# Optimization experiments

Hardware: AMD Instinct MI355X
Metric: run time of the kernel (lower is better)

## Reference

```python
import jax, jax.numpy as jnp
import numpy as np

B = 1          # batch
CAM = 6        # num cameras
HW = 256       # tokens per camera (16x16 latent)
N = CAM * HW   # 1536 image tokens
D = 1024       # model dim
H = 16         # heads
DH = 64        # dim_head
L = 4          # depth
V = 8192       # image token vocab
VC = 4096      # cond vocab
NC = 512       # num cond tokens
INNER = int(D * 4 * 2 / 3)  # 2730 GEGLU inner dim
SCALE = 8.0


def setup_inputs() -> dict:
    key = jax.random.key(0)
    ks = jax.random.split(key, 24)
    w = lambda k, shape: jax.random.normal(k, shape, jnp.float32) * 0.02
    inp = {
        'x': jax.random.randint(ks[0], (B * CAM, HW), 0, V),
        'cond_ids': jax.random.randint(ks[1], (B, NC), 0, VC),
        'token_emb': w(ks[2], (V, D)),
        'pos_emb': w(ks[3], (N, D)),
        'cond_token_emb': w(ks[4], (VC, D)),
        'cond_pos_emb': w(ks[5], (NC, D)),
        # self-attention (per layer, stacked on leading L axis)
        'sa_g': jnp.ones((L, D), jnp.float32),
        'sa_wq': w(ks[6], (L, D, H * DH)),
        'sa_wkv': w(ks[7], (L, D, 2 * H * DH)),
        'sa_null': jax.random.normal(ks[8], (L, 2, H, 1, DH), jnp.float32),
        'sa_qs': jnp.ones((L, DH), jnp.float32),
        'sa_ks': jnp.ones((L, DH), jnp.float32),
        'sa_wo': w(ks[9], (L, H * DH, D)),
        # cross-attention
        'ca_g': jnp.ones((L, D), jnp.float32),
        'ca_wq': w(ks[10], (L, D, H * DH)),
        'ca_wkv': w(ks[11], (L, D, 2 * H * DH)),
        'ca_null': jax.random.normal(ks[12], (L, 2, H, 1, DH), jnp.float32),
        'ca_qs': jnp.ones((L, DH), jnp.float32),
        'ca_ks': jnp.ones((L, DH), jnp.float32),
        'ca_wo': w(ks[13], (L, H * DH, D)),
        # GEGLU feedforward
        'ff_g1': jnp.ones((L, D), jnp.float32),
        'ff_w1': w(ks[14], (L, D, 2 * INNER)),
        'ff_g2': jnp.ones((L, INNER), jnp.float32),
        'ff_w2': w(ks[15], (L, INNER, D)),
        'final_g': jnp.ones((D,), jnp.float32),
        'w_logits': w(ks[16], (D, V)),
    }
    return inp


def _ln(x, g):
    m = jnp.mean(x, axis=-1, keepdims=True)
    v = jnp.var(x, axis=-1, keepdims=True)
    return (x - m) * jax.lax.rsqrt(v + 1e-5) * g


def _l2n(x):
    n = jnp.sqrt(jnp.sum(x * x, axis=-1, keepdims=True))
    return x / jnp.maximum(n, 1e-12)


def _attn(x, kv, g, wq, wkv, nkv, qs, ks_, wo):
    b, n, _ = x.shape
    xn = _ln(x, g)
    kv_in = xn if kv is None else kv  # cross-attn uses raw context (not normed)
    q = (xn @ wq) * SCALE  # matches torch (no-op after l2norm, kept faithful)
    k, v = jnp.split(kv_in @ wkv, 2, axis=-1)
    to_h = lambda t: t.reshape(b, -1, H, DH).transpose(0, 2, 1, 3)  # b h n d
    q, k, v = to_h(q), to_h(k), to_h(v)
    nk = jnp.broadcast_to(nkv[0], (b, H, 1, DH))
    nv = jnp.broadcast_to(nkv[1], (b, H, 1, DH))
    k = jnp.concatenate([nk, k], axis=2)
    v = jnp.concatenate([nv, v], axis=2)
    q = _l2n(q) * qs
    k = _l2n(k) * ks_
    sim = jnp.einsum('bhid,bhjd->bhij', q, k) * SCALE
    a = jax.nn.softmax(sim, axis=-1)
    o = jnp.einsum('bhij,bhjd->bhid', a, v)
    return o.transpose(0, 2, 1, 3).reshape(b, n, H * DH) @ wo


def _ff(x, g1, w1, g2, w2):
    h = _ln(x, g1) @ w1
    a, gate = jnp.split(h, 2, axis=-1)
    h = gate * jax.nn.gelu(a, approximate=False)  # GEGLU, exact gelu like torch
    return _ln(h, g2) @ w2


def reference(x, cond_ids, token_emb, pos_emb, cond_token_emb, cond_pos_emb,
              sa_g, sa_wq, sa_wkv, sa_null, sa_qs, sa_ks, sa_wo,
              ca_g, ca_wq, ca_wkv, ca_null, ca_qs, ca_ks, ca_wo,
              ff_g1, ff_w1, ff_g2, ff_w2, final_g, w_logits):
    h = token_emb[x].reshape(B, N, D) + pos_emb[:N]
    ctx = cond_token_emb[cond_ids] + cond_pos_emb[:NC]
    layer_params = (sa_g, sa_wq, sa_wkv, sa_null, sa_qs, sa_ks, sa_wo,
                    ca_g, ca_wq, ca_wkv, ca_null, ca_qs, ca_ks, ca_wo,
                    ff_g1, ff_w1, ff_g2, ff_w2)

    def body(h, p):
        (sg, swq, swkv, snull, sqs, sks, swo,
         cg, cwq, cwkv, cnull, cqs, cks, cwo,
         fg1, fw1, fg2, fw2) = p
        h = h + _attn(h, None, sg, swq, swkv, snull, sqs, sks, swo)
        h = h + _attn(h, ctx, cg, cwq, cwkv, cnull, cqs, cks, cwo)
        h = h + _ff(h, fg1, fw1, fg2, fw2)
        return h, None

    h, _ = jax.lax.scan(body, h, layer_params)
    h = _ln(h, final_g)  # TransformerBlocks.norm
    return h @ w_logits  # (B, N, V)
```

## Files before the change

### kernel.cpp

```cpp
#include <hip/hip_runtime.h>

typedef __attribute__((ext_vector_type(8))) short short8;
typedef __attribute__((ext_vector_type(4))) float f32x4;
typedef unsigned short u16;

#define N_TOK   1536
#define DMODEL  1024
#define NHEAD   16
#define DHEAD   64
#define NCTX    512
#define INNERD  2730
#define INNERP  2752
#define FF1P    5504
#define VOCAB   8192

__device__ __forceinline__ u16 f2b(float f) {
  union { float f; unsigned u; } v; v.f = f;
  unsigned r = (v.u >> 16) & 1u;
  return (u16)((v.u + 0x7fffu + r) >> 16);
}

__global__ __launch_bounds__(256) void conv_t(
    const float* __restrict__ in, u16* __restrict__ out,
    int K, int Nw, int Kpad, int Nbound, long long zin, long long zout)
{
  const float* inl = in + (size_t)blockIdx.z * zin;
  u16* outl = out + (size_t)blockIdx.z * zout;
  __shared__ float tile[64][65];
  int k0 = blockIdx.x * 64, n0 = blockIdx.y * 64;
  int tid = threadIdx.x;
  {
    int r = tid >> 4, c4 = (tid & 15) * 4;
#pragma unroll
    for (int j = 0; j < 4; j++) {
      int k = k0 + r + j * 16;
      float4 v = make_float4(0.f, 0.f, 0.f, 0.f);
      if (k < K && (n0 + c4) < Nw) v = *(const float4*)&inl[(size_t)k * Nw + n0 + c4];
      tile[r + j * 16][c4] = v.x; tile[r + j * 16][c4 + 1] = v.y;
      tile[r + j * 16][c4 + 2] = v.z; tile[r + j * 16][c4 + 3] = v.w;
    }
  }
  __syncthreads();
  {
    int nl = tid >> 2, kc = (tid & 3) * 16;
    int n = n0 + nl;
    if (n < Nbound) {
      u16 pk[16];
#pragma unroll
      for (int i = 0; i < 16; i++) pk[i] = f2b(tile[kc + i][nl]);
      u16* op = outl + (size_t)n * Kpad + k0 + kc;
      *(short8*)&op[0] = *(short8*)&pk[0];
      *(short8*)&op[8] = *(short8*)&pk[8];
    }
  }
}

__global__ void embed_img(const int* __restrict__ x, const float* __restrict__ temb,
                          const float* __restrict__ pemb, float* __restrict__ h) {
  int n = blockIdx.x; int tok = x[n]; int d4 = threadIdx.x;
  float4 a = *(const float4*)&temb[(size_t)tok * DMODEL + d4 * 4];
  float4 b = *(const float4*)&pemb[(size_t)n * DMODEL + d4 * 4];
  float4 o; o.x = a.x + b.x; o.y = a.y + b.y; o.z = a.z + b.z; o.w = a.w + b.w;
  *(float4*)&h[(size_t)n * DMODEL + d4 * 4] = o;
}

__global__ void embed_ctx(const int* __restrict__ ids, const float* __restrict__ temb,
                          const float* __restrict__ pemb, u16* __restrict__ ctxb) {
  int n = blockIdx.x; int tok = ids[n]; int d4 = threadIdx.x;
  float4 a = *(const float4*)&temb[(size_t)tok * DMODEL + d4 * 4];
  float4 b = *(const float4*)&pemb[(size_t)n * DMODEL + d4 * 4];
  u16* o = ctxb + (size_t)n * DMODEL + d4 * 4;
  o[0] = f2b(a.x + b.x); o[1] = f2b(a.y + b.y); o[2] = f2b(a.z + b.z); o[3] = f2b(a.w + b.w);
}

__global__ __launch_bounds__(256) void ln_bf16(
    const float* __restrict__ X, int ldin, const float* __restrict__ g,
    u16* __restrict__ Y, int ldout, int C, int Cpad)
{
  int row = blockIdx.x;
  const float* x = X + (size_t)row * ldin;
  float s = 0.f, sq = 0.f;
  for (int ci = threadIdx.x; ci < C; ci += 256) { float v = x[ci]; s += v; sq += v * v; }
#pragma unroll
  for (int m = 1; m < 64; m <<= 1) { s += __shfl_xor(s, m, 64); sq += __shfl_xor(sq, m, 64); }
  __shared__ float red[2][4];
  int w = threadIdx.x >> 6;
  if ((threadIdx.x & 63) == 0) { red[0][w] = s; red[1][w] = sq; }
  __syncthreads();
  s = red[0][0] + red[0][1] + red[0][2] + red[0][3];
  sq = red[1][0] + red[1][1] + red[1][2] + red[1][3];
  float mean = s / C;
  float var = sq / C - mean * mean;
  float rstd = rsqrtf(var + 1e-5f);
  u16* y = Y + (size_t)row * ldout;
  for (int ci = threadIdx.x; ci < C; ci += 256) y[ci] = f2b((x[ci] - mean) * rstd * g[ci]);
  for (int ci = C + threadIdx.x; ci < Cpad; ci += 256) y[ci] = 0;
}

template <int WMODE, int NSPLIT>
__global__ __launch_bounds__(256) void gemm_bt(
    const u16* __restrict__ A, const u16* __restrict__ Bt,
    float* __restrict__ C, int ldc, int M, int N, int K, int lda, int ldb)
{
  __shared__ __align__(16) short As[128 * 72];
  __shared__ __align__(16) short Bs[128 * 72];
  int tid = threadIdx.x;
  int bm = blockIdx.x, bn = blockIdx.y;
  int lane = tid & 63, w = tid >> 6;
  int wm = (w >> 1) * 64, wn = (w & 1) * 64;
  int rl = lane & 15, quad = lane >> 4;
  f32x4 acc[4][4];
#pragma unroll
  for (int i = 0; i < 4; i++)
#pragma unroll
    for (int j = 0; j < 4; j++) acc[i][j] = (f32x4)(0.f);
  const int rowA0 = bm * 128, rowB0 = bn * 128;
  int tiles = K >> 6;
  int t0 = (tiles * blockIdx.z) / NSPLIT, t1 = (tiles * (blockIdx.z + 1)) / NSPLIT;

  for (int kt = t0; kt < t1; kt++) {
    int k0 = kt * 64;
    __syncthreads();
#pragma unroll
    for (int i = 0; i < 4; i++) {
      int ch = tid + 256 * i;
      int r = ch >> 3, c8 = (ch & 7) * 8;
      *(short8*)&As[r * 72 + c8] = *(const short8*)(A + (size_t)(rowA0 + r) * lda + k0 + c8);
      *(short8*)&Bs[r * 72 + c8] = *(const short8*)(Bt + (size_t)(rowB0 + r) * ldb + k0 + c8);
    }
    __syncthreads();
#pragma unroll
    for (int kk = 0; kk < 64; kk += 32) {
      int kq = kk + quad * 8;
      short8 af[4], bfr[4];
#pragma unroll
      for (int t = 0; t < 4; t++) {
        af[t]  = *(const short8*)&As[(wm + t * 16 + rl) * 72 + kq];
        bfr[t] = *(const short8*)&Bs[(wn + t * 16 + rl) * 72 + kq];
      }
#pragma unroll
      for (int mt = 0; mt < 4; mt++)
#pragma unroll
        for (int nt = 0; nt < 4; nt++)
          acc[mt][nt] = __builtin_amdgcn_mfma_f32_16x16x32_bf16(af[mt], bfr[nt], acc[mt][nt], 0, 0, 0);
    }
  }
#pragma unroll
  for (int mt = 0; mt < 4; mt++)
#pragma unroll
    for (int nt = 0; nt < 4; nt++)
#pragma unroll
      for (int r = 0; r < 4; r++) {
        int row = rowA0 + wm + mt * 16 + quad * 4 + r;
        int col = rowB0 + wn + nt * 16 + rl;
        float* p = &C[(size_t)row * ldc + col];
        if (WMODE == 0) *p = acc[mt][nt][r];
        else if (WMODE == 1) *p += acc[mt][nt][r];
        else atomicAdd(p, acc[mt][nt][r]);
      }
}

__global__ __launch_bounds__(256) void prep_kv(
    const float* __restrict__ kvb,
    const float* __restrict__ nullkv, const float* __restrict__ ks,
    u16* __restrict__ Kn, u16* __restrict__ Vt, int Lk, int Lkp)
{
  int h = blockIdx.y, j0 = blockIdx.x * 64;
  int tid = threadIdx.x, w = tid >> 6, d = tid & 63;
  float ksd = ks[d];
#pragma unroll 4
  for (int r = 0; r < 16; r++) {
    int j = j0 + w * 16 + r;
    float k = 0.f;
    if (j == 0) k = nullkv[h * 64 + d];
    else if (j < Lk) k = kvb[(size_t)(j - 1) * 3072 + h * 64 + d];
    float ssq = k * k;
#pragma unroll
    for (int ms = 1; ms < 64; ms <<= 1) ssq += __shfl_xor(ssq, ms, 64);
    float kn = k * (1.0f / fmaxf(sqrtf(ssq), 1e-12f)) * ksd;
    Kn[((size_t)h * Lkp + j) * 64 + d] = f2b(kn);
  }
  __shared__ float tile[64][65];
  {
    int jl = tid >> 2, c16 = (tid & 3) * 16;
    int j = j0 + jl;
#pragma unroll
    for (int i4 = 0; i4 < 4; i4++) {
      float4 v = make_float4(0.f, 0.f, 0.f, 0.f);
      if (j == 0) v = *(const float4*)&nullkv[NHEAD * 64 + h * 64 + c16 + i4 * 4];
      else if (j < Lk) v = *(const float4*)&kvb[(size_t)(j - 1) * 3072 + 1024 + h * 64 + c16 + i4 * 4];
      tile[jl][c16 + i4 * 4] = v.x; tile[jl][c16 + i4 * 4 + 1] = v.y;
      tile[jl][c16 + i4 * 4 + 2] = v.z; tile[jl][c16 + i4 * 4 + 3] = v.w;
    }
  }
  __syncthreads();
  {
    int dd = tid >> 2, jc = (tid & 3) * 16;
    u16 pk[16];
#pragma unroll
    for (int i = 0; i < 16; i++) pk[i] = f2b(tile[jc + i][dd]);
    u16* op = Vt + ((size_t)h * 64 + dd) * Lkp + j0 + jc;
    *(short8*)&op[0] = *(short8*)&pk[0];
    *(short8*)&op[8] = *(short8*)&pk[8];
  }
}

__global__ __launch_bounds__(256) void attn_mfma(
    const float* __restrict__ qkv, const float* __restrict__ qs,
    const u16* __restrict__ Kn, const u16* __restrict__ Vt,
    float* __restrict__ Opar, float* __restrict__ Lpar, int Lkp, int nk)
{
  __shared__ __align__(16) u16 Kt[2][64 * 64];
  __shared__ __align__(16) u16 Vs[2][64 * 64];
  __shared__ __align__(16) short Ps[4 * 16 * 72];
  int tid = threadIdx.x, w = tid >> 6, lane = tid & 63;
  int rl = lane & 15, quad = lane >> 4;
  int b = blockIdx.x;
  int h = (b & 7) * 2 + ((b >> 3) & 1);
  int rest = b >> 4;
  int qg = rest >> 1, ks = rest & 1;
  int m0 = qg * 64 + w * 16;
  int t0 = (nk * ks) >> 1, t1 = (nk * (ks + 1)) >> 1;
  short* Pw = Ps + w * 16 * 72;

  short8 aq[2];
  {
    const float* qp = qkv + (size_t)(m0 + rl) * 3072 + h * 64;
    float qv[16];
    float ssq = 0.f;
#pragma unroll
    for (int cb = 0; cb < 2; cb++) {
      float4 v0 = *(const float4*)&qp[cb * 32 + quad * 8];
      float4 v1 = *(const float4*)&qp[cb * 32 + quad * 8 + 4];
      qv[cb * 8 + 0] = v0.x; qv[cb * 8 + 1] = v0.y; qv[cb * 8 + 2] = v0.z; qv[cb * 8 + 3] = v0.w;
      qv[cb * 8 + 4] = v1.x; qv[cb * 8 + 5] = v1.y; qv[cb * 8 + 6] = v1.z; qv[cb * 8 + 7] = v1.w;
      ssq += v0.x * v0.x + v0.y * v0.y + v0.z * v0.z + v0.w * v0.w;
      ssq += v1.x * v1.x + v1.y * v1.y + v1.z * v1.z + v1.w * v1.w;
    }
    ssq += __shfl_xor(ssq, 16, 64);
    ssq += __shfl_xor(ssq, 32, 64);
    float inv = 8.0f / fmaxf(sqrtf(ssq), 1e-12f);
    u16 pk[16];
#pragma unroll
    for (int cb = 0; cb < 2; cb++) {
      float4 s0 = *(const float4*)&qs[cb * 32 + quad * 8];
      float4 s1 = *(const float4*)&qs[cb * 32 + quad * 8 + 4];
      pk[cb * 8 + 0] = f2b(qv[cb * 8 + 0] * inv * s0.x);
      pk[cb * 8 + 1] = f2b(qv[cb * 8 + 1] * inv * s0.y);
      pk[cb * 8 + 2] = f2b(qv[cb * 8 + 2] * inv * s0.z);
      pk[cb * 8 + 3] = f2b(qv[cb * 8 + 3] * inv * s0.w);
      pk[cb * 8 + 4] = f2b(qv[cb * 8 + 4] * inv * s1.x);
      pk[cb * 8 + 5] = f2b(qv[cb * 8 + 5] * inv * s1.y);
      pk[cb * 8 + 6] = f2b(qv[cb * 8 + 6] * inv * s1.z);
      pk[cb * 8 + 7] = f2b(qv[cb * 8 + 7] * inv * s1.w);
    }
    aq[0] = *(short8*)&pk[0];
    aq[1] = *(short8*)&pk[8];
  }

  const u16* Kh = Kn + (size_t)h * Lkp * 64;
  const u16* Vh = Vt + (size_t)h * 64 * Lkp;

  int srow0 = w * 16 + (lane >> 3);
  int scol = (lane & 7) * 8;

  short8 stg[4];
  {
    int j0 = t0 * 64;
#pragma unroll
    for (int c = 0; c < 2; c++) {
      int row = srow0 + c * 8;
      stg[c]     = *(const short8*)(Kh + (size_t)(j0 + row) * 64 + scol);
      stg[2 + c] = *(const short8*)(Vh + (size_t)row * Lkp + j0 + scol);
    }
  }

  f32x4 oacc[4];
#pragma unroll
  for (int dt = 0; dt < 4; dt++) oacc[dt] = (f32x4)(0.f);
  float lrow[4] = {0.f, 0.f, 0.f, 0.f};

  for (int kt = t0; kt < t1; kt++) {
    int buf = kt & 1;
    u16* KtB = Kt[buf];
    u16* VsB = Vs[buf];
#pragma unroll
    for (int c = 0; c < 2; c++) {
      int row = srow0 + c * 8;
      int cs = scol ^ ((row & 7) * 8);
      *(short8*)&KtB[row * 64 + cs] = stg[c];
      *(short8*)&VsB[row * 64 + cs] = stg[2 + c];
    }
    if (kt + 1 < t1) {
      int j0 = (kt + 1) * 64;
#pragma unroll
      for (int c = 0; c < 2; c++) {
        int row = srow0 + c * 8;
        stg[c]     = *(const short8*)(Kh + (size_t)(j0 + row) * 64 + scol);
        stg[2 + c] = *(const short8*)(Vh + (size_t)row * Lkp + j0 + scol);
      }
    }
    __asm volatile("s_waitcnt lgkmcnt(0)" ::: "memory");
    __builtin_amdgcn_s_barrier();
    __asm volatile("" ::: "memory");

    f32x4 sacc[4];
#pragma unroll
    for (int nt = 0; nt < 4; nt++) sacc[nt] = (f32x4)(0.f);
#pragma unroll
    for (int kc = 0; kc < 2; kc++)
#pragma unroll
      for (int nt = 0; nt < 4; nt++) {
        short8 bkf = *(const short8*)&KtB[(nt * 16 + rl) * 64 + (((kc * 4 + quad) ^ (rl & 7)) * 8)];
        sacc[nt] = __builtin_amdgcn_mfma_f32_16x16x32_bf16(aq[kc], bkf, sacc[nt], 0, 0, 0);
      }

#pragma unroll
    for (int nt = 0; nt < 4; nt++)
#pragma unroll
      for (int r = 0; r < 4; r++) {
        float p = __expf(sacc[nt][r]);
        lrow[r] += p;
        Pw[(quad * 4 + r) * 72 + nt * 16 + rl] = (short)f2b(p);
      }
    __asm volatile("s_waitcnt lgkmcnt(0)" ::: "memory");
    short8 ap0 = *(const short8*)&Pw[rl * 72 + quad * 8];
    short8 ap1 = *(const short8*)&Pw[rl * 72 + 32 + quad * 8];
#pragma unroll
    for (int dt = 0; dt < 4; dt++) {
      short8 bv0 = *(const short8*)&VsB[(dt * 16 + rl) * 64 + ((quad ^ (rl & 7)) * 8)];
      short8 bv1 = *(const short8*)&VsB[(dt * 16 + rl) * 64 + (((4 + quad) ^ (rl & 7)) * 8)];
      oacc[dt] = __builtin_amdgcn_mfma_f32_16x16x32_bf16(ap0, bv0, oacc[dt], 0, 0, 0);
      oacc[dt] = __builtin_amdgcn_mfma_f32_16x16x32_bf16(ap1, bv1, oacc[dt], 0, 0, 0);
    }
    __asm volatile("" ::: "memory");
  }

#pragma unroll
  for (int r = 0; r < 4; r++) {
#pragma unroll
    for (int ms = 1; ms < 16; ms <<= 1) lrow[r] += __shfl_xor(lrow[r], ms, 64);
  }
  float* Op = Opar + ((size_t)ks * N_TOK + m0) * DMODEL + h * 64;
#pragma unroll
  for (int dt = 0; dt < 4; dt++)
#pragma unroll
    for (int r = 0; r < 4; r++)
      Op[(size_t)(quad * 4 + r) * DMODEL + dt * 16 + rl] = oacc[dt][r];
  if (rl == 0) {
#pragma unroll
    for (int r = 0; r < 4; r++)
      Lpar[((size_t)ks * N_TOK + m0 + quad * 4 + r) * 16 + h] = lrow[r];
  }
}

__global__ __launch_bounds__(256) void attn_fin(
    const float* __restrict__ Opar, const float* __restrict__ Lpar,
    u16* __restrict__ Ob, float pad)
{
  int m = blockIdx.x, t = threadIdx.x;
  int c = t * 4, hh = t >> 4;
  float l = Lpar[(size_t)m * 16 + hh] + Lpar[(size_t)(N_TOK + m) * 16 + hh] - pad;
  float inv = 1.0f / l;
  float4 a = *(const float4*)(Opar + (size_t)m * DMODEL + c);
  float4 d = *(const float4*)(Opar + (size_t)(N_TOK + m) * DMODEL + c);
  u16* op = Ob + (size_t)m * DMODEL + c;
  op[0] = f2b((a.x + d.x) * inv);
  op[1] = f2b((a.y + d.y) * inv);
  op[2] = f2b((a.z + d.z) * inv);
  op[3] = f2b((a.w + d.w) * inv);
}

__global__ __launch_bounds__(256) void geglu_ln(
    const float* __restrict__ h1, const float* __restrict__ g2, u16* __restrict__ Y)
{
  int row = blockIdx.x;
  const float* p = h1 + (size_t)row * FF1P;
  float act[11];
  float s = 0.f, sq = 0.f;
#pragma unroll
  for (int t = 0; t < 11; t++) {
    int i = threadIdx.x + t * 256;
    float v = 0.f;
    if (i < INNERD) {
      float a = p[i], gate = p[INNERD + i];
      float ge = 0.5f * a * (1.0f + erff(a * 0.70710678118654752f));
      v = gate * ge;
    }
    act[t] = v; s += v; sq += v * v;
  }
#pragma unroll
  for (int m = 1; m < 64; m <<= 1) { s += __shfl_xor(s, m, 64); sq += __shfl_xor(sq, m, 64); }
  __shared__ float red[2][4];
  int w = threadIdx.x >> 6;
  if ((threadIdx.x & 63) == 0) { red[0][w] = s; red[1][w] = sq; }
  __syncthreads();
  s = red[0][0] + red[0][1] + red[0][2] + red[0][3];
  sq = red[1][0] + red[1][1] + red[1][2] + red[1][3];
  float mean = s / INNERD;
  float var = sq / INNERD - mean * mean;
  float rstd = rsqrtf(var + 1e-5f);
  u16* y = Y + (size_t)row * INNERP;
#pragma unroll
  for (int t = 0; t < 11; t++) {
    int i = threadIdx.x + t * 256;
    if (i < INNERD) y[i] = f2b((act[t] - mean) * rstd * g2[i]);
  }
  if (threadIdx.x < INNERP - INNERD) y[INNERD + threadIdx.x] = 0;
}

extern "C" void kernel_launch(void* const* d_in, const int* in_sizes, int n_in,
                              void* d_out, int out_size, void* d_ws, size_t ws_size,
                              hipStream_t stream) {
  const int*   x        = (const int*)d_in[0];
  const int*   cond_ids = (const int*)d_in[1];
  const float* token_emb      = (const float*)d_in[2];
  const float* pos_emb        = (const float*)d_in[3];
  const float* cond_token_emb = (const float*)d_in[4];
  const float* cond_pos_emb   = (const float*)d_in[5];
  const float* sa_g   = (const float*)d_in[6];
  const float* sa_wq  = (const float*)d_in[7];
  const float* sa_wkv = (const float*)d_in[8];
  const float* sa_null= (const float*)d_in[9];
  const float* sa_qs  = (const float*)d_in[10];
  const float* sa_ks  = (const float*)d_in[11];
  const float* sa_wo  = (const float*)d_in[12];
  const float* ca_g   = (const float*)d_in[13];
  const float* ca_wq  = (const float*)d_in[14];
  const float* ca_wkv = (const float*)d_in[15];
  const float* ca_null= (const float*)d_in[16];
  const float* ca_qs  = (const float*)d_in[17];
  const float* ca_ks  = (const float*)d_in[18];
  const float* ca_wo  = (const float*)d_in[19];
  const float* ff_g1  = (const float*)d_in[20];
  const float* ff_w1  = (const float*)d_in[21];
  const float* ff_g2  = (const float*)d_in[22];
  const float* ff_w2  = (const float*)d_in[23];
  const float* final_g  = (const float*)d_in[24];
  const float* w_logits = (const float*)d_in[25];

  char* base = (char*)d_ws; size_t off = 0;
  auto alloc = [&](size_t bytes) -> void* {
    void* r = base + off; off = (off + bytes + 255) & ~(size_t)255; return r;
  };
  u16* sa_qkv_t = (u16*)alloc((size_t)4 * 3072 * 1024 * 2);
  u16* sa_wo_t  = (u16*)alloc((size_t)4 * 1024 * 1024 * 2);
  u16* ca_wq_t  = (u16*)alloc((size_t)4 * 1024 * 1024 * 2);
  u16* ca_wkv_t = (u16*)alloc((size_t)4 * 2048 * 1024 * 2);
  u16* ca_wo_t  = (u16*)alloc((size_t)4 * 1024 * 1024 * 2);
  u16* ff_w1_t  = (u16*)alloc((size_t)4 * FF1P * 1024 * 2);
  u16* ff_w2_t  = (u16*)alloc((size_t)4 * 1024 * INNERP * 2);
  u16* logits_t = (u16*)alloc((size_t)VOCAB * 1024 * 2);
  float* h    = (float*)alloc((size_t)N_TOK * DMODEL * 4);
  u16*   ctxb = (u16*)alloc((size_t)NCTX * DMODEL * 2);
  u16*   xnb  = (u16*)alloc((size_t)N_TOK * INNERP * 2);
  float* qkv  = (float*)alloc((size_t)N_TOK * 3072 * 4);
  u16*   Kn   = (u16*)alloc((size_t)NHEAD * 1600 * 64 * 2);
  u16*   Vt   = (u16*)alloc((size_t)NHEAD * 64 * 1600 * 2);
  u16*   ob   = (u16*)alloc((size_t)N_TOK * DMODEL * 2);
  float* h1   = (float*)alloc((size_t)N_TOK * FF1P * 4);
  float* Opar = (float*)h1;
  float* Lpar = Opar + (size_t)2 * N_TOK * DMODEL;
  (void)ws_size; (void)in_sizes; (void)n_in; (void)out_size;

  conv_t<<<dim3(16, 16, 4), 256, 0, stream>>>(sa_wq,  sa_qkv_t,              1024, 1024, 1024, 1024, 1024LL*1024, 3072LL*1024);
  conv_t<<<dim3(16, 32, 4), 256, 0, stream>>>(sa_wkv, sa_qkv_t + 1024*1024,  1024, 2048, 1024, 2048, 1024LL*2048, 3072LL*1024);
  conv_t<<<dim3(16, 16, 4), 256, 0, stream>>>(sa_wo,  sa_wo_t,               1024, 1024, 1024, 1024, 1024LL*1024, 1024LL*1024);
  conv_t<<<dim3(16, 16, 4), 256, 0, stream>>>(ca_wq,  ca_wq_t,               1024, 1024, 1024, 1024, 1024LL*1024, 1024LL*1024);
  conv_t<<<dim3(16, 32, 4), 256, 0, stream>>>(ca_wkv, ca_wkv_t,              1024, 2048, 1024, 2048, 1024LL*2048, 2048LL*1024);
  conv_t<<<dim3(16, 16, 4), 256, 0, stream>>>(ca_wo,  ca_wo_t,               1024, 1024, 1024, 1024, 1024LL*1024, 1024LL*1024);
  conv_t<<<dim3(16, 86, 4), 256, 0, stream>>>(ff_w1,  ff_w1_t,               1024, 5460, 1024, FF1P, 1024LL*5460, (long long)FF1P*1024);
  conv_t<<<dim3(43, 16, 4), 256, 0, stream>>>(ff_w2,  ff_w2_t,               INNERD, 1024, INNERP, 1024, (long long)INNERD*1024, 1024LL*INNERP);
  conv_t<<<dim3(16, 128, 1), 256, 0, stream>>>(w_logits, logits_t,           1024, VOCAB, 1024, VOCAB, 0, 0);

  embed_img<<<dim3(N_TOK), dim3(256), 0, stream>>>(x, token_emb, pos_emb, h);
  embed_ctx<<<dim3(NCTX), dim3(256), 0, stream>>>(cond_ids, cond_token_emb, cond_pos_emb, ctxb);

  for (int l = 0; l < 4; l++) {
    const u16* sqkv = sa_qkv_t + (size_t)l * 3072 * 1024;
    const u16* swo  = sa_wo_t  + (size_t)l * 1024 * 1024;
    const u16* cwq  = ca_wq_t  + (size_t)l * 1024 * 1024;
    const u16* cwkv = ca_wkv_t + (size_t)l * 2048 * 1024;
    const u16* cwo  = ca_wo_t  + (size_t)l * 1024 * 1024;
    const u16* fw1  = ff_w1_t  + (size_t)l * FF1P * 1024;
    const u16* fw2  = ff_w2_t  + (size_t)l * 1024 * INNERP;

    ln_bf16<<<dim3(N_TOK), dim3(256), 0, stream>>>(h, DMODEL, sa_g + l * DMODEL, xnb, DMODEL, DMODEL, DMODEL);
    gemm_bt<0, 1><<<dim3(12, 24, 1), dim3(256), 0, stream>>>(xnb, sqkv, qkv, 3072, N_TOK, 3072, 1024, 1024, 1024);
    prep_kv<<<dim3(25, NHEAD), dim3(256), 0, stream>>>(qkv + 1024, sa_null + l * 2048, sa_ks + l * 64, Kn, Vt, 1537, 1600);
    attn_mfma<<<dim3(768), dim3(256), 0, stream>>>(qkv, sa_qs + l * 64, Kn, Vt, Opar, Lpar, 1600, 25);
    attn_fin<<<dim3(N_TOK), dim3(256), 0, stream>>>(Opar, Lpar, ob, 63.0f);
    gemm_bt<2, 4><<<dim3(12, 8, 4), dim3(256), 0, stream>>>(ob, swo, h, 1024, N_TOK, 1024, 1024, 1024, 1024);

    ln_bf16<<<dim3(N_TOK), dim3(256), 0, stream>>>(h, DMODEL, ca_g + l * DMODEL, xnb, DMODEL, DMODEL, DMODEL);
    hipMemsetAsync(qkv, 0, (size_t)N_TOK * 3072 * 4, stream);
    gemm_bt<2, 4><<<dim3(12, 8, 4), dim3(256), 0, stream>>>(xnb, cwq, qkv, 3072, N_TOK, 1024, 1024, 1024, 1024);
    gemm_bt<2, 4><<<dim3(4, 16, 4), dim3(256), 0, stream>>>(ctxb, cwkv, qkv + 1024, 3072, NCTX, 2048, 1024, 1024, 1024);
    prep_kv<<<dim3(9, NHEAD), dim3(256), 0, stream>>>(qkv + 1024, ca_null + l * 2048, ca_ks + l * 64, Kn, Vt, 513, 576);
    attn_mfma<<<dim3(768), dim3(256), 0, stream>>>(qkv, ca_qs + l * 64, Kn, Vt, Opar, Lpar, 576, 9);
    attn_fin<<<dim3(N_TOK), dim3(256), 0, stream>>>(Opar, Lpar, ob, 63.0f);
    gemm_bt<2, 4><<<dim3(12, 8, 4), dim3(256), 0, stream>>>(ob, cwo, h, 1024, N_TOK, 1024, 1024, 1024, 1024);

    ln_bf16<<<dim3(N_TOK), dim3(256), 0, stream>>>(h, DMODEL, ff_g1 + l * DMODEL, xnb, DMODEL, DMODEL, DMODEL);
    gemm_bt<0, 1><<<dim3(12, 43, 1), dim3(256), 0, stream>>>(xnb, fw1, h1, FF1P, N_TOK, FF1P, 1024, 1024, 1024);
    geglu_ln<<<dim3(N_TOK), dim3(256), 0, stream>>>(h1, ff_g2 + l * INNERD, xnb);
    gemm_bt<2, 4><<<dim3(12, 8, 4), dim3(256), 0, stream>>>(xnb, fw2, h, 1024, N_TOK, 1024, INNERP, INNERP, INNERP);
  }

  ln_bf16<<<dim3(N_TOK), dim3(256), 0, stream>>>(h, DMODEL, final_g, xnb, DMODEL, DMODEL, DMODEL);
  gemm_bt<0, 1><<<dim3(12, 64, 1), dim3(256), 0, stream>>>(xnb, logits_t, (float*)d_out, VOCAB, N_TOK, VOCAB, 1024, 1024, 1024);
}
```

Measured before the change: 1.688 ms.

## Load GEMM tiles directly to LDS and swizzle workgroups across XCDs

Replaces the register-staged global-to-shared copy in the bf16 GEMM with direct global_load_lds 16-byte loads. The LDS tile loses its padding, so the layout becomes 64 columns wide, and the next K tile is issued after compute instead of before it. It also remaps workgroup IDs so that consecutive tiles land on the same XCD, for better L2 locality. The unpadded LDS layout can cause bank conflicts on the fragment reads, and with a single buffer there is little real overlap.

Result: slower. 1.745 ms (+3.4%).

```diff
diff --git a/kernel.cpp b/kernel.cpp
--- a/kernel.cpp
+++ b/kernel.cpp
@@ -18,6 +18,12 @@
   union { float f; unsigned u; } v; v.f = f;
   unsigned r = (v.u >> 16) & 1u;
   return (u16)((v.u + 0x7fffu + r) >> 16);
+}
+
+__device__ __forceinline__ void gload16(const u16* g, u16* l) {
+  __builtin_amdgcn_global_load_lds(
+      (const __attribute__((address_space(1))) void*)g,
+      (__attribute__((address_space(3))) void*)l, 16, 0, 0);
 }
 
 __global__ __launch_bounds__(256) void conv_t(
@@ -102,10 +108,17 @@
     const u16* __restrict__ A, const u16* __restrict__ Bt,
     float* __restrict__ C, int ldc, int M, int N, int K, int lda, int ldb)
 {
-  __shared__ __align__(16) short As[128 * 72];
-  __shared__ __align__(16) short Bs[128 * 72];
+  __shared__ __align__(16) u16 As[128 * 64];
+  __shared__ __align__(16) u16 Bs[128 * 64];
   int tid = threadIdx.x;
-  int bm = blockIdx.x, bn = blockIdx.y;
+  int gx = gridDim.x;
+  int nwg = gx * gridDim.y;
+  int id = blockIdx.x + gx * blockIdx.y;
+  int q = nwg >> 3, r = nwg & 7;
+  int xcd = id & 7, jj = id >> 3;
+  int swz = (xcd < r ? xcd * (q + 1) : r * (q + 1) + (xcd - r) * q) + jj;
+  int bm = swz % gx, bn = swz / gx;
+
   int lane = tid & 63, w = tid >> 6;
   int wm = (w >> 1) * 64, wn = (w & 1) * 64;
   int rl = lane & 15, quad = lane >> 4;
@@ -118,16 +131,23 @@
   int tiles = K >> 6;
   int t0 = (tiles * blockIdx.z) / NSPLIT, t1 = (tiles * (blockIdx.z + 1)) / NSPLIT;
 
+  int srow = lane >> 3;
+  int scol = (lane & 7) * 8;
+
+#define GEMM_STAGE(k0)                                                        \
+  {                                                                           \
+    _Pragma("unroll")                                                         \
+    for (int i = 0; i < 4; i++) {                                             \
+      int rg = w * 32 + i * 8;                                                \
+      gload16(A  + (size_t)(rowA0 + rg + srow) * lda + (k0) + scol, &As[rg * 64]); \
+      gload16(Bt + (size_t)(rowB0 + rg + srow) * ldb + (k0) + scol, &Bs[rg * 64]); \
+    }                                                                         \
+  }
+
+  GEMM_STAGE(t0 * 64);
+
   for (int kt = t0; kt < t1; kt++) {
-    int k0 = kt * 64;
-    __syncthreads();
-#pragma unroll
-    for (int i = 0; i < 4; i++) {
-      int ch = tid + 256 * i;
-      int r = ch >> 3, c8 = (ch & 7) * 8;
-      *(short8*)&As[r * 72 + c8] = *(const short8*)(A + (size_t)(rowA0 + r) * lda + k0 + c8);
-      *(short8*)&Bs[r * 72 + c8] = *(const short8*)(Bt + (size_t)(rowB0 + r) * ldb + k0 + c8);
-    }
+    __asm volatile("s_waitcnt vmcnt(0)" ::: "memory");
     __syncthreads();
 #pragma unroll
     for (int kk = 0; kk < 64; kk += 32) {
@@ -135,8 +155,8 @@
       short8 af[4], bfr[4];
 #pragma unroll
       for (int t = 0; t < 4; t++) {
-        af[t]  = *(const short8*)&As[(wm + t * 16 + rl) * 72 + kq];
-        bfr[t] = *(const short8*)&Bs[(wn + t * 16 + rl) * 72 + kq];
+        af[t]  = *(const short8*)&As[(wm + t * 16 + rl) * 64 + kq];
+        bfr[t] = *(const short8*)&Bs[(wn + t * 16 + rl) * 64 + kq];
       }
 #pragma unroll
       for (int mt = 0; mt < 4; mt++)
@@ -144,19 +164,23 @@
         for (int nt = 0; nt < 4; nt++)
           acc[mt][nt] = __builtin_amdgcn_mfma_f32_16x16x32_bf16(af[mt], bfr[nt], acc[mt][nt], 0, 0, 0);
     }
-  }
+    __syncthreads();
+    if (kt + 1 < t1) GEMM_STAGE((kt + 1) * 64);
+  }
+#undef GEMM_STAGE
+
 #pragma unroll
   for (int mt = 0; mt < 4; mt++)
 #pragma unroll
     for (int nt = 0; nt < 4; nt++)
 #pragma unroll
-      for (int r = 0; r < 4; r++) {
-        int row = rowA0 + wm + mt * 16 + quad * 4 + r;
+      for (int r2 = 0; r2 < 4; r2++) {
+        int row = rowA0 + wm + mt * 16 + quad * 4 + r2;
         int col = rowB0 + wn + nt * 16 + rl;
         float* p = &C[(size_t)row * ldc + col];
-        if (WMODE == 0) *p = acc[mt][nt][r];
-        else if (WMODE == 1) *p += acc[mt][nt][r];
-        else atomicAdd(p, acc[mt][nt][r]);
+        if (WMODE == 0) *p = acc[mt][nt][r2];
+        else if (WMODE == 1) *p += acc[mt][nt][r2];
+        else atomicAdd(p, acc[mt][nt][r2]);
       }
 }
 
```
